# Kernel tuning notes

Measured on AMD Instinct MI355X. Metric: run time of the kernel, lower is better.

The kernel has to match this reference:

```python
import jax, jax.numpy as jnp
import numpy as np

N = 10  # input_size
P = 6   # part_num


def setup_inputs() -> dict:
    key = jax.random.key(0)
    X = jax.random.uniform(key, (N,), dtype=jnp.float32)
    # Learned params as initialized in __init__ (cast to float32)
    a = jnp.tile(jnp.linspace(0.0, 1.0, P, dtype=jnp.float32)[None, :], (N, 1))  # [N,P]
    b = jnp.full((N, P), 1.0 / P ** 1.5, dtype=jnp.float32)                       # [N,P]
    y = jnp.full((P ** (N - 1), P), 0.5, dtype=jnp.float32)                       # rule consequents
    return {"X": X, "a": a, "b": b, "y": y}


def reference(X, a, b, y):
    # Gaussian memberships, one row per input feature: [N, P]
    h_ = jnp.exp(-((a - X[:, None]) ** 2) / (2.0 * b ** 2))
    # Sequential outer-product chain over the N feature rows -> flat [P**N]
    h = h_[0]
    for i in range(1, N):  # fixed trace-time loop over feature dim (N is a hyperparam)
        h = (h[:, None] * h_[i][None, :]).reshape(-1)
    # Weighted average of rule consequents (scalar)
    num = jnp.sum(h * y.reshape(-1))
    den = jnp.sum(h)
    return num / den
```

## Files before the change

### kernel.cpp

```cpp
#include <hip/hip_runtime.h>
#include <math.h>


#define NF 10
#define PP 6
#define HI 7776
#define HI4 1944
#define BLK 256

typedef float fvec4 __attribute__((ext_vector_type(4)));


__global__ void tsk_prep(const float* __restrict__ X,
                         const float* __restrict__ a,
                         const float* __restrict__ b,
                         float* __restrict__ ws) {
    __shared__ float h[NF][PP];
    const int tid = threadIdx.x;
    if (tid < NF * PP) {
        const int k = tid / PP;
        const float d = a[tid] - X[k];
        const float bb = b[tid];
        h[k][tid % PP] = expf(-(d * d) / (2.0f * bb * bb));
    }
    __syncthreads();
    float* __restrict__ Whi = ws + 8;
    float* __restrict__ Wlo = ws + 8 + HI;
    for (int r = tid; r < HI; r += blockDim.x) {
        int t = r;
        const int d4 = t % 6; t /= 6;
        const int d3 = t % 6; t /= 6;
        const int d2 = t % 6; t /= 6;
        const int d1 = t % 6; t /= 6;
        const int d0 = t;
        Whi[r] = h[0][d0] * h[1][d1] * h[2][d2] * h[3][d3] * h[4][d4];
        Wlo[r] = h[5][d0] * h[6][d1] * h[7][d2] * h[8][d3] * h[9][d4];
    }
    if (tid == 0) {
        float den = 1.0f;
        for (int k = 0; k < NF; ++k) {
            float s = 0.0f;
            for (int i = 0; i < PP; ++i) s += h[k][i];
            den *= s;
        }
        ws[0] = den;
    }
}

__global__ __launch_bounds__(BLK) void tsk_dot(const float* __restrict__ y,
                                               float* __restrict__ ws) {
    const fvec4* __restrict__ wlo4 = (const fvec4*)(ws + 8 + HI);
    float* __restrict__ partial = ws + 8 + 2 * HI;
    const int r = blockIdx.x;
    const fvec4* __restrict__ yrow = (const fvec4*)(y + (size_t)r * HI);
    const int t = threadIdx.x;

    float acc = 0.0f;
    #pragma unroll
    for (int k = 0; k < 7; ++k) {
        const int c = t + k * BLK;
        const fvec4 yv = __builtin_nontemporal_load(yrow + c);
        const fvec4 wv = wlo4[c];
        acc += yv.x * wv.x + yv.y * wv.y + yv.z * wv.z + yv.w * wv.w;
    }
    {
        const int c = t + 7 * BLK;
        if (c < HI4) {
            const fvec4 yv = __builtin_nontemporal_load(yrow + c);
            const fvec4 wv = wlo4[c];
            acc += yv.x * wv.x + yv.y * wv.y + yv.z * wv.z + yv.w * wv.w;
        }
    }

    #pragma unroll
    for (int off = 32; off > 0; off >>= 1) acc += __shfl_down(acc, off, 64);
    __shared__ float ssum[BLK / 64];
    const int lane = t & 63;
    const int wave = t >> 6;
    if (lane == 0) ssum[wave] = acc;
    __syncthreads();
    if (t == 0) {
        float s = 0.0f;
        #pragma unroll
        for (int w = 0; w < BLK / 64; ++w) s += ssum[w];
        partial[r] = s;
    }
}

__global__ __launch_bounds__(1024) void tsk_reduce(const float* __restrict__ ws,
                                                   float* __restrict__ out) {
    const float* __restrict__ Whi = ws + 8;
    const float* __restrict__ partial = ws + 8 + 2 * HI;
    const int t = threadIdx.x;

    float acc = 0.0f;
    #pragma unroll
    for (int k = 0; k < 8; ++k) {
        const int r = t + k * 1024;
        if (r < HI) acc += partial[r] * Whi[r];
    }
    #pragma unroll
    for (int off = 32; off > 0; off >>= 1) acc += __shfl_down(acc, off, 64);
    __shared__ float ssum[16];
    const int lane = t & 63;
    const int wave = t >> 6;
    if (lane == 0) ssum[wave] = acc;
    __syncthreads();
    if (t == 0) {
        float s = 0.0f;
        #pragma unroll
        for (int w = 0; w < 16; ++w) s += ssum[w];
        out[0] = s / ws[0];
    }
}

extern "C" void kernel_launch(void* const* d_in, const int* in_sizes, int n_in,
                              void* d_out, int out_size, void* d_ws, size_t ws_size,
                              hipStream_t stream) {
    const float* X = (const float*)d_in[0];
    const float* a = (const float*)d_in[1];
    const float* b = (const float*)d_in[2];
    const float* y = (const float*)d_in[3];
    float* out = (float*)d_out;
    float* ws  = (float*)d_ws;

    tsk_prep<<<1, 1024, 0, stream>>>(X, a, b, ws);
    tsk_dot<<<HI, BLK, 0, stream>>>(y, ws);
    tsk_reduce<<<1, 1024, 0, stream>>>(ws, out);
}
```

Measured before the change: 314.9 us.

## Fuse membership prep into dot kernel with per-block LDS weights and two rows per block

```diff
diff --git a/kernel.cpp b/kernel.cpp
--- a/kernel.cpp
+++ b/kernel.cpp
@@ -7,110 +7,127 @@
 #define HI 7776
 #define HI4 1944
 #define BLK 256
+#define ROWS 2
 
 typedef float fvec4 __attribute__((ext_vector_type(4)));
 
 
-__global__ void tsk_prep(const float* __restrict__ X,
-                         const float* __restrict__ a,
-                         const float* __restrict__ b,
-                         float* __restrict__ ws) {
+__device__ __forceinline__ float memb(const float* X, const float* a,
+                                      const float* b, int idx) {
+    const int k = idx / PP;
+    const float d = a[idx] - X[k];
+    const float bb = b[idx];
+    return __expf(-(d * d) / (2.0f * bb * bb));
+}
+
+__global__ __launch_bounds__(BLK) void tsk_fused(const float* __restrict__ X,
+                                                 const float* __restrict__ a,
+                                                 const float* __restrict__ b,
+                                                 const float* __restrict__ y,
+                                                 float* __restrict__ ws) {
     __shared__ float h[NF][PP];
-    const int tid = threadIdx.x;
-    if (tid < NF * PP) {
-        const int k = tid / PP;
-        const float d = a[tid] - X[k];
-        const float bb = b[tid];
-        h[k][tid % PP] = expf(-(d * d) / (2.0f * bb * bb));
+    __shared__ float wlo[HI];
+    __shared__ float ssum[BLK / 64][ROWS];
+    const int t = threadIdx.x;
+
+    if (t < NF * PP) h[t / PP][t % PP] = memb(X, a, b, t);
+    __syncthreads();
+
+    for (int c = t; c < HI; c += BLK) {
+        int u = c;
+        const int d9 = u % 6; u /= 6;
+        const int d8 = u % 6; u /= 6;
+        const int d7 = u % 6; u /= 6;
+        const int d6 = u % 6; u /= 6;
+        const int d5 = u;
+        wlo[c] = h[5][d5] * h[6][d6] * h[7][d7] * h[8][d8] * h[9][d9];
     }
     __syncthreads();
-    float* __restrict__ Whi = ws + 8;
-    float* __restrict__ Wlo = ws + 8 + HI;
-    for (int r = tid; r < HI; r += blockDim.x) {
-        int t = r;
-        const int d4 = t % 6; t /= 6;
-        const int d3 = t % 6; t /= 6;
-        const int d2 = t % 6; t /= 6;
-        const int d1 = t % 6; t /= 6;
-        const int d0 = t;
-        Whi[r] = h[0][d0] * h[1][d1] * h[2][d2] * h[3][d3] * h[4][d4];
-        Wlo[r] = h[5][d0] * h[6][d1] * h[7][d2] * h[8][d3] * h[9][d4];
-    }
-    if (tid == 0) {
-        float den = 1.0f;
-        for (int k = 0; k < NF; ++k) {
-            float s = 0.0f;
-            for (int i = 0; i < PP; ++i) s += h[k][i];
-            den *= s;
+
+    const fvec4* __restrict__ wlo4 = (const fvec4*)wlo;
+    const int r0 = blockIdx.x * ROWS;
+
+    float accs[ROWS];
+    for (int i = 0; i < ROWS; ++i) {
+        const fvec4* __restrict__ yrow = (const fvec4*)(y + (size_t)(r0 + i) * HI);
+        float acc = 0.0f;
+        #pragma unroll
+        for (int k = 0; k < 7; ++k) {
+            const int c = t + k * BLK;
+            const fvec4 yv = __builtin_nontemporal_load(yrow + c);
+            const fvec4 wv = wlo4[c];
+            acc += yv.x * wv.x + yv.y * wv.y + yv.z * wv.z + yv.w * wv.w;
         }
-        ws[0] = den;
-    }
-}
-
-__global__ __launch_bounds__(BLK) void tsk_dot(const float* __restrict__ y,
-                                               float* __restrict__ ws) {
-    const fvec4* __restrict__ wlo4 = (const fvec4*)(ws + 8 + HI);
-    float* __restrict__ partial = ws + 8 + 2 * HI;
-    const int r = blockIdx.x;
-    const fvec4* __restrict__ yrow = (const fvec4*)(y + (size_t)r * HI);
-    const int t = threadIdx.x;
-
-    float acc = 0.0f;
-    #pragma unroll
-    for (int k = 0; k < 7; ++k) {
-        const int c = t + k * BLK;
-        const fvec4 yv = __builtin_nontemporal_load(yrow + c);
-        const fvec4 wv = wlo4[c];
-        acc += yv.x * wv.x + yv.y * wv.y + yv.z * wv.z + yv.w * wv.w;
-    }
-    {
         const int c = t + 7 * BLK;
         if (c < HI4) {
             const fvec4 yv = __builtin_nontemporal_load(yrow + c);
             const fvec4 wv = wlo4[c];
             acc += yv.x * wv.x + yv.y * wv.y + yv.z * wv.z + yv.w * wv.w;
         }
+        accs[i] = acc;
     }
 
     #pragma unroll
+    for (int i = 0; i < ROWS; ++i) {
+        #pragma unroll
+        for (int off = 32; off > 0; off >>= 1)
+            accs[i] += __shfl_down(accs[i], off, 64);
+    }
+    const int lane = t & 63;
+    const int wave = t >> 6;
+    if (lane == 0) {
+        #pragma unroll
+        for (int i = 0; i < ROWS; ++i) ssum[wave][i] = accs[i];
+    }
+    __syncthreads();
+    if (t < ROWS) {
+        float s = 0.0f;
+        #pragma unroll
+        for (int w = 0; w < BLK / 64; ++w) s += ssum[w][t];
+        int u = r0 + t;
+        const int d4 = u % 6; u /= 6;
+        const int d3 = u % 6; u /= 6;
+        const int d2 = u % 6; u /= 6;
+        const int d1 = u % 6; u /= 6;
+        const int d0 = u;
+        const float whi = h[0][d0] * h[1][d1] * h[2][d2] * h[3][d3] * h[4][d4];
+        ws[r0 + t] = s * whi;
+    }
+}
+
+__global__ __launch_bounds__(1024) void tsk_reduce(const float* __restrict__ X,
+                                                   const float* __restrict__ a,
+                                                   const float* __restrict__ b,
+                                                   const float* __restrict__ ws,
+                                                   float* __restrict__ out) {
+    __shared__ float h[NF * PP];
+    __shared__ float ssum[16];
+    const int t = threadIdx.x;
+    if (t < NF * PP) h[t] = memb(X, a, b, t);
+
+    float acc = 0.0f;
+    #pragma unroll
+    for (int k = 0; k < 8; ++k) {
+        const int r = t + k * 1024;
+        if (r < HI) acc += ws[r];
+    }
+    #pragma unroll
     for (int off = 32; off > 0; off >>= 1) acc += __shfl_down(acc, off, 64);
-    __shared__ float ssum[BLK / 64];
     const int lane = t & 63;
     const int wave = t >> 6;
     if (lane == 0) ssum[wave] = acc;
     __syncthreads();
     if (t == 0) {
-        float s = 0.0f;
+        float num = 0.0f;
         #pragma unroll
-        for (int w = 0; w < BLK / 64; ++w) s += ssum[w];
-        partial[r] = s;
-    }
-}
-
-__global__ __launch_bounds__(1024) void tsk_reduce(const float* __restrict__ ws,
-                                                   float* __restrict__ out) {
-    const float* __restrict__ Whi = ws + 8;
-    const float* __restrict__ partial = ws + 8 + 2 * HI;
-    const int t = threadIdx.x;
-
-    float acc = 0.0f;
-    #pragma unroll
-    for (int k = 0; k < 8; ++k) {
-        const int r = t + k * 1024;
-        if (r < HI) acc += partial[r] * Whi[r];
-    }
-    #pragma unroll
-    for (int off = 32; off > 0; off >>= 1) acc += __shfl_down(acc, off, 64);
-    __shared__ float ssum[16];
-    const int lane = t & 63;
-    const int wave = t >> 6;
-    if (lane == 0) ssum[wave] = acc;
-    __syncthreads();
-    if (t == 0) {
-        float s = 0.0f;
-        #pragma unroll
-        for (int w = 0; w < 16; ++w) s += ssum[w];
-        out[0] = s / ws[0];
+        for (int w = 0; w < 16; ++w) num += ssum[w];
+        float den = 1.0f;
+        for (int k = 0; k < NF; ++k) {
+            float s = 0.0f;
+            for (int i = 0; i < PP; ++i) s += h[k * PP + i];
+            den *= s;
+        }
+        out[0] = num / den;
     }
 }
 
@@ -124,7 +141,6 @@
     float* out = (float*)d_out;
     float* ws  = (float*)d_ws;
 
-    tsk_prep<<<1, 1024, 0, stream>>>(X, a, b, ws);
-    tsk_dot<<<HI, BLK, 0, stream>>>(y, ws);
-    tsk_reduce<<<1, 1024, 0, stream>>>(ws, out);
+    tsk_fused<<<HI / ROWS, BLK, 0, stream>>>(X, a, b, y, ws);
+    tsk_reduce<<<1, 1024, 0, stream>>>(X, a, b, ws, out);
 }
```

After: 312.3 us. Within noise of the previous version (-0.8%).
